# Optimization experiments

Hardware: AMD Instinct MI355X
Metric: run time of the kernel (lower is better)

Reference implementation:

```python
import jax, jax.numpy as jnp
import numpy as np

N_PEP, N_MHC, N_TCR = 20000, 5000, 100000
EMB, HID = 128, 256
E_PM, E_MT = 200000, 400000
B = 50000


def setup_inputs() -> dict:
    key = jax.random.key(0)
    ks = jax.random.split(key, 30)
    f32 = jnp.float32

    def w(k, shape, fan_in):
        # torch Linear default: U(-1/sqrt(fan_in), 1/sqrt(fan_in))
        lim = 1.0 / np.sqrt(fan_in)
        return jax.random.uniform(k, shape, dtype=f32, minval=-lim, maxval=lim)

    inp = {
        # embedding tables (learned params)
        "emb_pep": jax.random.normal(ks[0], (N_PEP, EMB), dtype=f32),
        "emb_mhc": jax.random.normal(ks[1], (N_MHC, EMB), dtype=f32),
        "emb_tcr": jax.random.normal(ks[2], (N_TCR, EMB), dtype=f32),
        # edge lists (src=edge_index[0], dst=edge_index[1])
        "src_pm": jax.random.randint(ks[3], (E_PM,), 0, N_PEP, dtype=jnp.int32),
        "dst_pm": jax.random.randint(ks[4], (E_PM,), 0, N_MHC, dtype=jnp.int32),
        "src_mt": jax.random.randint(ks[5], (E_MT,), 0, N_MHC, dtype=jnp.int32),
        "dst_mt": jax.random.randint(ks[6], (E_MT,), 0, N_TCR, dtype=jnp.int32),
        # triplet pack indices
        "pack_pep": jax.random.randint(ks[7], (B,), 0, N_PEP, dtype=jnp.int32),
        "pack_mhc": jax.random.randint(ks[8], (B,), 0, N_MHC, dtype=jnp.int32),
        "pack_tcr": jax.random.randint(ks[9], (B,), 0, N_TCR, dtype=jnp.int32),
        # SAGEConv params: Wl (aggregated neighbors, with bias), Wr (root, no bias)
        # layer 1: pep->mhc (src 128, dst 128); mhc->tcr (src 128, dst 128)
        "l1_pm_Wl": w(ks[10], (HID, EMB), EMB), "l1_pm_bl": w(ks[11], (HID,), EMB),
        "l1_pm_Wr": w(ks[12], (HID, EMB), EMB),
        "l1_mt_Wl": w(ks[13], (HID, EMB), EMB), "l1_mt_bl": w(ks[14], (HID,), EMB),
        "l1_mt_Wr": w(ks[15], (HID, EMB), EMB),
        # layer 2: pep->mhc (src 128, dst 256); mhc->tcr (src 256, dst 256)
        "l2_pm_Wl": w(ks[16], (HID, EMB), EMB), "l2_pm_bl": w(ks[17], (HID,), EMB),
        "l2_pm_Wr": w(ks[18], (HID, HID), HID),
        "l2_mt_Wl": w(ks[19], (HID, HID), HID), "l2_mt_bl": w(ks[20], (HID,), HID),
        "l2_mt_Wr": w(ks[21], (HID, HID), HID),
        # proj_pep and head MLP
        "proj_W": w(ks[22], (HID, EMB), EMB), "proj_b": w(ks[23], (HID,), EMB),
        "head_W1": w(ks[24], (HID, 3 * HID), 3 * HID), "head_b1": w(ks[25], (HID,), 3 * HID),
        "head_W2": w(ks[26], (1, HID), HID), "head_b2": w(ks[27], (1,), HID),
    }
    return inp


def _sage(x_src, x_dst, src, dst, Wl, bl, Wr, n_dst):
    # SAGEConv(mean): lin_l(mean_{j in N(i)} x_src[j]) + lin_r(x_dst[i])
    msg = jax.ops.segment_sum(x_src[src], dst, num_segments=n_dst)  # [n_dst, d_src]
    cnt = jax.ops.segment_sum(jnp.ones((src.shape[0],), x_src.dtype), dst, num_segments=n_dst)
    mean = msg / jnp.maximum(cnt, 1.0)[:, None]
    return mean @ Wl.T + bl + x_dst @ Wr.T


def reference(emb_pep, emb_mhc, emb_tcr,
              src_pm, dst_pm, src_mt, dst_mt,
              pack_pep, pack_mhc, pack_tcr,
              l1_pm_Wl, l1_pm_bl, l1_pm_Wr, l1_mt_Wl, l1_mt_bl, l1_mt_Wr,
              l2_pm_Wl, l2_pm_bl, l2_pm_Wr, l2_mt_Wl, l2_mt_bl, l2_mt_Wr,
              proj_W, proj_b, head_W1, head_b1, head_W2, head_b2):
    relu = jax.nn.relu
    # layer 1 (HeteroConv reads all relations from the same input dict)
    mhc1 = relu(_sage(emb_pep, emb_mhc, src_pm, dst_pm, l1_pm_Wl, l1_pm_bl, l1_pm_Wr, N_MHC))
    tcr1 = relu(_sage(emb_mhc, emb_tcr, src_mt, dst_mt, l1_mt_Wl, l1_mt_bl, l1_mt_Wr, N_TCR))
    # layer 2 ('pep' is never a destination, so it keeps its embedding)
    mhc2 = relu(_sage(emb_pep, mhc1, src_pm, dst_pm, l2_pm_Wl, l2_pm_bl, l2_pm_Wr, N_MHC))
    tcr2 = relu(_sage(mhc1, tcr1, src_mt, dst_mt, l2_mt_Wl, l2_mt_bl, l2_mt_Wr, N_TCR))
    # projections + triplet gather (dropout disabled: inference)
    hp = (emb_pep @ proj_W.T + proj_b)[pack_pep]  # [B, HID]
    hm = mhc2[pack_mhc]
    ht = tcr2[pack_tcr]
    z = jnp.concatenate([hp, hm, ht], axis=-1)  # [B, 3*HID]
    hidden = relu(z @ head_W1.T + head_b1)
    logits = hidden @ head_W2.T + head_b2
    return logits.squeeze(-1)
```

## Files before the change

### kernel.cpp

```cpp
#include <hip/hip_runtime.h>

constexpr int NPEP = 20000, NMHC = 5000, NTCR = 100000;
constexpr int EPM = 200000, EMT = 400000, BB = 50000;
constexpr int MAXU = 50000;

typedef __attribute__((ext_vector_type(8))) short bf16x8;
typedef __attribute__((ext_vector_type(4))) float f32x4;

__device__ inline ushort f2bf(float x) {
    union { float f; unsigned u; } v; v.f = x;
    unsigned r = (v.u + 0x7FFF + ((v.u >> 16) & 1)) >> 16;
    return (ushort)r;
}
__device__ inline float bf2f(ushort b) {
    union { unsigned u; float f; } t; t.u = ((unsigned)b) << 16; return t.f;
}
__device__ inline void bf2x2(unsigned u, float& a, float& b) {
    union { unsigned x; float f; } t1, t2;
    t1.x = u << 16; t2.x = u & 0xffff0000u;
    a = t1.f; b = t2.f;
}
__device__ inline ushort4 f4bf(float4 v) {
    return make_ushort4(f2bf(v.x), f2bf(v.y), f2bf(v.z), f2bf(v.w));
}

__global__ __launch_bounds__(256) void prep_kernel(
    int* __restrict__ ibz,
    const float4* __restrict__ Wr1f, ushort4* __restrict__ Wr1_b,
    const float4* __restrict__ Wr2f, ushort4* __restrict__ Wr2_b,
    const float* __restrict__ head_W1, ushort4* __restrict__ W1b_b, ushort4* __restrict__ W1c_b,
    const float* __restrict__ l1_pm_Wl, const float* __restrict__ l1_pm_Wr,
    const float* __restrict__ l1_mt_Wl, ushort* __restrict__ Wcat1_b,
    const float* __restrict__ l2_pm_Wl, const float* __restrict__ l2_pm_Wr,
    const float* __restrict__ l2_mt_Wl, ushort* __restrict__ Wcat2_b,
    const float4* __restrict__ emb_mhc, ushort* __restrict__ Acat1,
    const float* __restrict__ proj_W, const float* __restrict__ proj_b,
    ushort* __restrict__ Wcomp_b, float* __restrict__ bp) {
    __shared__ float red[128];
    const int b = blockIdx.x, tid = threadIdx.x;
    if (b < 303) {
        int i = b * 256 + tid;
        if (i < 77500) ((int4*)ibz)[i] = make_int4(0, 0, 0, 0);
    } else if (b < 335) {
        int i = (b - 303) * 256 + tid;
        if (i < 8192) Wr1_b[i] = f4bf(Wr1f[i]);
    } else if (b < 399) {
        int i = (b - 335) * 256 + tid;
        if (i < 16384) Wr2_b[i] = f4bf(Wr2f[i]);
    } else if (b < 463) {
        int i = (b - 399) * 256 + tid;
        if (i < 16384) {
            int n = i >> 6, k4 = (i & 63) * 4;
            float4 v = *(const float4*)(head_W1 + (size_t)n * 768 + 256 + k4);
            W1b_b[i] = f4bf(v);
        }
    } else if (b < 527) {
        int i = (b - 463) * 256 + tid;
        if (i < 16384) {
            int n = i >> 6, k4 = (i & 63) * 4;
            float4 v = *(const float4*)(head_W1 + (size_t)n * 768 + 512 + k4);
            W1c_b[i] = f4bf(v);
        }
    } else if (b < 1039) {
        int idx = (b - 527) * 256 + tid;
        if (idx < 131072) {
            int r = idx >> 8, k = idx & 255;
            float v;
            if (r < 256) v = (k < 128) ? l1_pm_Wl[r * 128 + k] : l1_pm_Wr[r * 128 + (k - 128)];
            else         v = (k < 128) ? 0.f : l1_mt_Wl[(r - 256) * 128 + (k - 128)];
            Wcat1_b[idx] = f2bf(v);
        }
    } else if (b < 1807) {
        int idx = (b - 1039) * 256 + tid;
        if (idx < 196608) {
            int r = idx / 384, k = idx - r * 384;
            float v;
            if (r < 256) v = (k < 128) ? l2_pm_Wl[r * 128 + k] : l2_pm_Wr[r * 256 + (k - 128)];
            else         v = (k < 128) ? 0.f : l2_mt_Wl[(r - 256) * 256 + (k - 128)];
            Wcat2_b[idx] = f2bf(v);
        }
    } else if (b < 2432) {
        int i4 = (b - 1807) * 256 + tid;
        if (i4 < 160000) {
            int r = i4 >> 5, c4 = (i4 & 31) * 4;
            *(ushort4*)(Acat1 + (size_t)r * 256 + 128 + c4) = f4bf(emb_mhc[i4]);
        }
    } else {
        int i = b - 2432;
        const float* w1row = head_W1 + (size_t)i * 768;
        if (tid < 128) {
            float acc = 0.f;
            for (int k = 0; k < 256; k++) acc += w1row[k] * proj_W[k * 128 + tid];
            Wcomp_b[i * 128 + tid] = f2bf(acc);
            float pb = w1row[2 * tid] * proj_b[2 * tid] + w1row[2 * tid + 1] * proj_b[2 * tid + 1];
            red[tid] = pb;
        }
        __syncthreads();
        if (tid < 64) { red[tid] += red[tid + 64]; }
        __syncthreads();
        if (tid < 32) { red[tid] += red[tid + 32]; }
        __syncthreads();
        if (tid == 0) {
            float s = 0.f;
            for (int j = 0; j < 32; j++) s += red[j];
            bp[i] = s;
        }
    }
}

__global__ void hist2_kernel(const int* __restrict__ dst_pm, const int* __restrict__ dst_mt,
                             const int* __restrict__ pack_tcr,
                             int* __restrict__ deg_pm, int* __restrict__ deg_mt,
                             int* __restrict__ mark) {
    int t = blockIdx.x * blockDim.x + threadIdx.x;
    if (t < EPM) atomicAdd(&deg_pm[dst_pm[t]], 1);
    else if (t < EPM + EMT) atomicAdd(&deg_mt[dst_mt[t - EPM]], 1);
    else if (t < EPM + EMT + BB) mark[pack_tcr[t - EPM - EMT]] = 1;
}

__global__ __launch_bounds__(256) void blocksum2_kernel(const int* __restrict__ deg_pm,
                                                        const int* __restrict__ deg_mt,
                                                        const int* __restrict__ mark,
                                                        int* __restrict__ bsum_pm,
                                                        int* __restrict__ bsum_mt,
                                                        int* __restrict__ bsum_mk) {
    __shared__ int red[256];
    const int tid = threadIdx.x;
    const int* deg; int n, bi; int* bsum;
    if (blockIdx.x < 5) { deg = deg_pm; n = NMHC; bi = blockIdx.x; bsum = bsum_pm; }
    else if (blockIdx.x < 103) { deg = deg_mt; n = NTCR; bi = blockIdx.x - 5; bsum = bsum_mt; }
    else { deg = mark; n = NTCR; bi = blockIdx.x - 103; bsum = bsum_mk; }
    const int base = bi * 1024;
    int s = 0;
#pragma unroll
    for (int j = 0; j < 4; j++) {
        int i = base + tid + j * 256;
        if (i < n) s += deg[i];
    }
    red[tid] = s;
    __syncthreads();
    for (int off = 128; off > 0; off >>= 1) {
        if (tid < off) red[tid] += red[tid + off];
        __syncthreads();
    }
    if (tid == 0) bsum[bi] = red[0];
}

__global__ __launch_bounds__(128) void scanb2_kernel(int* __restrict__ bsum_pm,
                                                     int* __restrict__ bsum_mt,
                                                     int* __restrict__ bsum_mk) {
    __shared__ int s[128];
    const int tid = threadIdx.x;
    int* bsum = (blockIdx.x == 0) ? bsum_pm : ((blockIdx.x == 1) ? bsum_mt : bsum_mk);
    const int nb = (blockIdx.x == 0) ? 5 : 98;
    int v = (tid < nb) ? bsum[tid] : 0;
    s[tid] = v;
    __syncthreads();
    for (int off = 1; off < 128; off <<= 1) {
        int t = (tid >= off) ? s[tid - off] : 0;
        __syncthreads();
        s[tid] += t;
        __syncthreads();
    }
    if (tid < nb) bsum[tid] = (tid > 0) ? s[tid - 1] : 0;
    if (tid == 0) bsum[nb] = s[nb - 1];
}

__global__ __launch_bounds__(256) void emit2_kernel(const int* __restrict__ deg_pm,
                                                    const int* __restrict__ deg_mt,
                                                    const int* __restrict__ mark,
                                                    const int* __restrict__ bsum_pm,
                                                    const int* __restrict__ bsum_mt,
                                                    const int* __restrict__ bsum_mk,
                                                    int* __restrict__ rp_pm, float* __restrict__ cnt_pm,
                                                    int* __restrict__ rp_mt, float* __restrict__ cnt_mt,
                                                    int* __restrict__ list) {
    __shared__ int tsum[256];
    const int tid = threadIdx.x;
    const int* deg; const int* bsum; int* rp; float* cnt; int n, nb, bi, mode;
    if (blockIdx.x < 5) { deg = deg_pm; bsum = bsum_pm; rp = rp_pm; cnt = cnt_pm; n = NMHC; nb = 5; bi = blockIdx.x; mode = 0; }
    else if (blockIdx.x < 103) { deg = deg_mt; bsum = bsum_mt; rp = rp_mt; cnt = cnt_mt; n = NTCR; nb = 98; bi = blockIdx.x - 5; mode = 0; }
    else { deg = mark; bsum = bsum_mk; rp = nullptr; cnt = nullptr; n = NTCR; nb = 98; bi = blockIdx.x - 103; mode = 1; }
    const int i0 = bi * 1024 + tid * 4;
    int4 v = make_int4(0, 0, 0, 0);
    if (i0 + 3 < n) v = *(const int4*)(deg + i0);
    else if (i0 < n) {
        int t[4] = {0, 0, 0, 0};
        for (int j = 0; j < 4 && i0 + j < n; j++) t[j] = deg[i0 + j];
        v = make_int4(t[0], t[1], t[2], t[3]);
    }
    int s = v.x + v.y + v.z + v.w;
    tsum[tid] = s;
    __syncthreads();
    for (int off = 1; off < 256; off <<= 1) {
        int t = (tid >= off) ? tsum[tid - off] : 0;
        __syncthreads();
        tsum[tid] += t;
        __syncthreads();
    }
    int ex = ((tid > 0) ? tsum[tid - 1] : 0) + bsum[bi];
    if (mode == 0) {
        if (i0 + 3 < n) {
            int r1 = ex + v.x, r2 = r1 + v.y, r3 = r2 + v.z;
            *(int4*)(rp + i0) = make_int4(ex, r1, r2, r3);
            *(float4*)(cnt + i0) = make_float4((float)v.x, (float)v.y, (float)v.z, (float)v.w);
        } else if (i0 < n) {
            int r = ex;
            int vv[4] = {v.x, v.y, v.z, v.w};
            for (int j = 0; j < 4 && i0 + j < n; j++) {
                rp[i0 + j] = r;
                cnt[i0 + j] = (float)vv[j];
                r += vv[j];
            }
        }
        if (bi == 0 && tid == 0) rp[n] = bsum[nb];
    } else {
        int p = ex;
        int vv[4] = {v.x, v.y, v.z, v.w};
#pragma unroll
        for (int j = 0; j < 4; j++) {
            if (i0 + j < n && vv[j]) list[p++] = i0 + j;
        }
    }
}

__global__ void fill2_kernel(const int* __restrict__ src_pm, const int* __restrict__ dst_pm,
                             const int* __restrict__ src_mt, const int* __restrict__ dst_mt,
                             const int* __restrict__ rp_pm, int* __restrict__ cur_pm, int* __restrict__ csr_pm,
                             const int* __restrict__ rp_mt, int* __restrict__ cur_mt, int* __restrict__ csr_mt) {
    int t = blockIdx.x * blockDim.x + threadIdx.x;
    if (t < EPM) {
        int d = dst_pm[t];
        int pos = atomicAdd(&cur_pm[d], 1);
        csr_pm[rp_pm[d] + pos] = src_pm[t];
    } else if (t < EPM + EMT) {
        int t2 = t - EPM;
        int d = dst_mt[t2];
        int pos = atomicAdd(&cur_mt[d], 1);
        csr_mt[rp_mt[d] + pos] = src_mt[t2];
    }
}

__global__ __launch_bounds__(256) void gatherpm_kernel(const int* __restrict__ rp,
                                                       const int* __restrict__ csr_src,
                                                       const float* __restrict__ X,
                                                       ushort* __restrict__ A1, ushort* __restrict__ A2,
                                                       int n) {
    const int tid = threadIdx.x;
    const int r = blockIdx.x * 8 + (tid >> 5);
    const int lane = tid & 31;
    if (r >= n) return;
    const int e0 = rp[r], e1 = rp[r + 1];
    float4 s = make_float4(0.f, 0.f, 0.f, 0.f);
    for (int e = e0; e < e1; e++) {
        const int sidx = csr_src[e];
        float4 v = ((const float4*)(X + (long)sidx * 128))[lane];
        s.x += v.x; s.y += v.y; s.z += v.z; s.w += v.w;
    }
    float sc = 1.f / fmaxf((float)(e1 - e0), 1.f);
    ushort4 o = make_ushort4(f2bf(s.x * sc), f2bf(s.y * sc), f2bf(s.z * sc), f2bf(s.w * sc));
    *(ushort4*)(A1 + (size_t)r * 256 + lane * 4) = o;
    *(ushort4*)(A2 + (size_t)r * 384 + lane * 4) = o;
}

template <int K, int NB0, bool RELU0, bool G2>
__global__ __launch_bounds__(256, 2) void mfma_fused_kernel(
    int M, const ushort* __restrict__ A, const ushort* __restrict__ W,
    const float* __restrict__ bias,
    ushort* __restrict__ out0, int s0, ushort* __restrict__ out1) {
    constexpr int RS = 40;
    __shared__ ushort Als[128 * RS];
    __shared__ ushort Wls[128 * RS];
    const int tid = threadIdx.x;
    const int m0 = blockIdx.x * 128, n0 = blockIdx.y * 128;
    const int lane = tid & 63, w = tid >> 6;
    const int wm = w >> 1, wn = w & 1;
    const int m16 = lane & 15, q = lane >> 4;

    f32x4 acc[4][4] = {};

    for (int k0 = 0; k0 < K; k0 += 32) {
        bf16x8 a_st[2], w_st[2];
#pragma unroll
        for (int r = 0; r < 2; r++) {
            int chunk = tid + r * 256;
            int row = chunk >> 2, off = (chunk & 3) * 8;
            int ga = min(m0 + row, M - 1);
            a_st[r] = *(const bf16x8*)(A + (size_t)ga * K + k0 + off);
            w_st[r] = *(const bf16x8*)(W + (size_t)(n0 + row) * K + k0 + off);
        }
        __syncthreads();
#pragma unroll
        for (int r = 0; r < 2; r++) {
            int chunk = tid + r * 256;
            int row = chunk >> 2, off = (chunk & 3) * 8;
            *(bf16x8*)(&Als[row * RS + off]) = a_st[r];
            *(bf16x8*)(&Wls[row * RS + off]) = w_st[r];
        }
        __syncthreads();
        bf16x8 af[4], bf[4];
#pragma unroll
        for (int t = 0; t < 4; t++) {
            af[t] = *(const bf16x8*)(&Als[(wm * 64 + t * 16 + m16) * RS + q * 8]);
            bf[t] = *(const bf16x8*)(&Wls[(wn * 64 + t * 16 + m16) * RS + q * 8]);
        }
#pragma unroll
        for (int mt = 0; mt < 4; mt++)
#pragma unroll
            for (int nt = 0; nt < 4; nt++)
                acc[mt][nt] = __builtin_amdgcn_mfma_f32_16x16x32_bf16(af[mt], bf[nt], acc[mt][nt], 0, 0, 0);
    }

    const bool g1 = G2 && ((int)blockIdx.y >= NB0);
#pragma unroll
    for (int mt = 0; mt < 4; mt++) {
#pragma unroll
        for (int i = 0; i < 4; i++) {
            int row = m0 + wm * 64 + mt * 16 + q * 4 + i;
            if (row >= M) continue;
#pragma unroll
            for (int nt = 0; nt < 4; nt++) {
                int col = n0 + wn * 64 + nt * 16 + m16;
                float v = acc[mt][nt][i];
                if (!g1) {
                    v += bias[col];
                    if (RELU0) v = fmaxf(v, 0.f);
                    out0[(size_t)row * s0 + col] = f2bf(v);
                } else {
                    out1[(size_t)row * 256 + (col - NB0 * 128)] = f2bf(v);
                }
            }
        }
    }
}

__global__ __launch_bounds__(256, 3) void tcrall_kernel(
    const int* __restrict__ nrowsp, const int* __restrict__ list,
    const int* __restrict__ rp, const int* __restrict__ csr_src,
    const ushort* __restrict__ Z1, const ushort* __restrict__ Z2,
    const float* __restrict__ emb_tcr,
    const ushort* __restrict__ Wr1, const ushort* __restrict__ Wr2,
    const ushort* __restrict__ W1c,
    const float* __restrict__ bl1, const float* __restrict__ bl2,
    ushort* __restrict__ Ht) {
    constexpr int RS1 = 136;
    constexpr int RS2 = 264;
    __shared__ ushort B[32 * RS2];
    __shared__ ushort A1[32 * RS2];
    __shared__ ushort A2[32 * RS2];
    __shared__ int origs[32];
    const int tid = threadIdx.x;
    const int M = nrowsp[0];
    const int m0 = blockIdx.x * 32;
    if (m0 >= M) return;
    const int lane = tid & 63, w = tid >> 6;
    const int m16 = lane & 15, q = lane >> 4;

    if (tid < 32) origs[tid] = list[min(m0 + tid, M - 1)];

#pragma unroll
    for (int r = 0; r < 4; r++) {
        int chunk = tid + r * 256;
        int row = chunk >> 5, c4 = (chunk & 31) * 4;
        int grow = list[min(m0 + row, M - 1)];
        float4 v = *(const float4*)(emb_tcr + (size_t)grow * 128 + c4);
        *(ushort4*)(&B[row * RS1 + c4]) = f4bf(v);
    }

    {
        const int g = tid >> 5, gl = tid & 31;
        for (int rr = g; rr < 32; rr += 8) {
            int cr = min(m0 + rr, M - 1);
            int orig = list[cr];
            int e0 = rp[orig], e1 = rp[orig + 1];
            float s1[8] = {}, s2[8] = {};
            for (int e = e0; e < e1; e++) {
                int sidx = csr_src[e];
                uint4 u1 = *(const uint4*)(Z1 + (size_t)sidx * 256 + gl * 8);
                uint4 u2 = *(const uint4*)(Z2 + (size_t)sidx * 256 + gl * 8);
                float a, b;
                bf2x2(u1.x, a, b); s1[0] += a; s1[1] += b;
                bf2x2(u1.y, a, b); s1[2] += a; s1[3] += b;
                bf2x2(u1.z, a, b); s1[4] += a; s1[5] += b;
                bf2x2(u1.w, a, b); s1[6] += a; s1[7] += b;
                bf2x2(u2.x, a, b); s2[0] += a; s2[1] += b;
                bf2x2(u2.y, a, b); s2[2] += a; s2[3] += b;
                bf2x2(u2.z, a, b); s2[4] += a; s2[5] += b;
                bf2x2(u2.w, a, b); s2[6] += a; s2[7] += b;
            }
            float es = 1.f / fmaxf((float)(e1 - e0), 1.f);
            uint4 w1, w2;
            w1.x = (unsigned)f2bf(s1[0] * es) | ((unsigned)f2bf(s1[1] * es) << 16);
            w1.y = (unsigned)f2bf(s1[2] * es) | ((unsigned)f2bf(s1[3] * es) << 16);
            w1.z = (unsigned)f2bf(s1[4] * es) | ((unsigned)f2bf(s1[5] * es) << 16);
            w1.w = (unsigned)f2bf(s1[6] * es) | ((unsigned)f2bf(s1[7] * es) << 16);
            w2.x = (unsigned)f2bf(s2[0] * es) | ((unsigned)f2bf(s2[1] * es) << 16);
            w2.y = (unsigned)f2bf(s2[2] * es) | ((unsigned)f2bf(s2[3] * es) << 16);
            w2.z = (unsigned)f2bf(s2[4] * es) | ((unsigned)f2bf(s2[5] * es) << 16);
            w2.w = (unsigned)f2bf(s2[6] * es) | ((unsigned)f2bf(s2[7] * es) << 16);
            *(uint4*)(&A1[rr * RS2 + gl * 8]) = w1;
            *(uint4*)(&A2[rr * RS2 + gl * 8]) = w2;
        }
    }
    __syncthreads();

    {
        f32x4 acc[2][4] = {};
        for (int k0 = 0; k0 < 128; k0 += 32) {
            bf16x8 af[2], bf[4];
#pragma unroll
            for (int t = 0; t < 2; t++)
                af[t] = *(const bf16x8*)(&B[(t * 16 + m16) * RS1 + k0 + q * 8]);
#pragma unroll
            for (int t = 0; t < 4; t++)
                bf[t] = *(const bf16x8*)(Wr1 + (size_t)(w * 64 + t * 16 + m16) * 128 + k0 + q * 8);
#pragma unroll
            for (int mt = 0; mt < 2; mt++)
#pragma unroll
                for (int nt = 0; nt < 4; nt++)
                    acc[mt][nt] = __builtin_amdgcn_mfma_f32_16x16x32_bf16(af[mt], bf[nt], acc[mt][nt], 0, 0, 0);
        }
        __syncthreads();
#pragma unroll
        for (int mt = 0; mt < 2; mt++)
#pragma unroll
            for (int i = 0; i < 4; i++) {
                int lr = mt * 16 + q * 4 + i;
#pragma unroll
                for (int nt = 0; nt < 4; nt++) {
                    int col = w * 64 + nt * 16 + m16;
                    float v = acc[mt][nt][i] + bl1[col] + bf2f(A1[lr * RS2 + col]);
                    B[lr * RS2 + col] = f2bf(fmaxf(v, 0.f));
                }
            }
    }
    __syncthreads();

    {
        f32x4 acc[2][4] = {};
        for (int k0 = 0; k0 < 256; k0 += 32) {
            bf16x8 af[2], bf[4];
#pragma unroll
            for (int t = 0; t < 2; t++)
                af[t] = *(const bf16x8*)(&B[(t * 16 + m16) * RS2 + k0 + q * 8]);
#pragma unroll
            for (int t = 0; t < 4; t++)
                bf[t] = *(const bf16x8*)(Wr2 + (size_t)(w * 64 + t * 16 + m16) * 256 + k0 + q * 8);
#pragma unroll
            for (int mt = 0; mt < 2; mt++)
#pragma unroll
                for (int nt = 0; nt < 4; nt++)
                    acc[mt][nt] = __builtin_amdgcn_mfma_f32_16x16x32_bf16(af[mt], bf[nt], acc[mt][nt], 0, 0, 0);
        }
        __syncthreads();
#pragma unroll
        for (int mt = 0; mt < 2; mt++)
#pragma unroll
            for (int i = 0; i < 4; i++) {
                int lr = mt * 16 + q * 4 + i;
#pragma unroll
                for (int nt = 0; nt < 4; nt++) {
                    int col = w * 64 + nt * 16 + m16;
                    float v = acc[mt][nt][i] + bl2[col] + bf2f(A2[lr * RS2 + col]);
                    B[lr * RS2 + col] = f2bf(fmaxf(v, 0.f));
                }
            }
    }
    __syncthreads();

    {
        f32x4 acc[2][4] = {};
        for (int k0 = 0; k0 < 256; k0 += 32) {
            bf16x8 af[2], bf[4];
#pragma unroll
            for (int t = 0; t < 2; t++)
                af[t] = *(const bf16x8*)(&B[(t * 16 + m16) * RS2 + k0 + q * 8]);
#pragma unroll
            for (int t = 0; t < 4; t++)
                bf[t] = *(const bf16x8*)(W1c + (size_t)(w * 64 + t * 16 + m16) * 256 + k0 + q * 8);
#pragma unroll
            for (int mt = 0; mt < 2; mt++)
#pragma unroll
                for (int nt = 0; nt < 4; nt++)
                    acc[mt][nt] = __builtin_amdgcn_mfma_f32_16x16x32_bf16(af[mt], bf[nt], acc[mt][nt], 0, 0, 0);
        }
        __syncthreads();
#pragma unroll
        for (int mt = 0; mt < 2; mt++)
#pragma unroll
            for (int i = 0; i < 4; i++) {
                int lr = mt * 16 + q * 4 + i;
#pragma unroll
                for (int nt = 0; nt < 4; nt++) {
                    int col = w * 64 + nt * 16 + m16;
                    B[lr * RS2 + col] = f2bf(acc[mt][nt][i]);
                }
            }
    }
    __syncthreads();

#pragma unroll
    for (int r = 0; r < 4; r++) {
        int chunk = tid + r * 256;
        int row = chunk >> 5, c8 = (chunk & 31) * 8;
        if (m0 + row < M)
            *(uint4*)(Ht + (size_t)origs[row] * 256 + c8) = *(const uint4*)(&B[row * RS2 + c8]);
    }
}

template <int K, bool HASB, bool AF32>
__global__ __launch_bounds__(256, 2) void mfma_out_kernel(
    int M, const void* __restrict__ Av, const ushort* __restrict__ W,
    const float* __restrict__ bias, ushort* __restrict__ out) {
    constexpr int RS = 40;
    __shared__ ushort Als[128 * RS];
    __shared__ ushort Wls[128 * RS];
    const int tid = threadIdx.x;
    const int m0 = blockIdx.x * 128, n0 = blockIdx.y * 128;
    const int lane = tid & 63, w = tid >> 6;
    const int wm = w >> 1, wn = w & 1;
    const int m16 = lane & 15, q = lane >> 4;

    f32x4 acc[4][4] = {};

    for (int k0 = 0; k0 < K; k0 += 32) {
        bf16x8 a_st[2], w_st[2];
#pragma unroll
        for (int r = 0; r < 2; r++) {
            int chunk = tid + r * 256;
            int row = chunk >> 2, off = (chunk & 3) * 8;
            int ga = min(m0 + row, M - 1);
            if constexpr (AF32) {
                const float* Af = (const float*)Av;
                float4 f0 = *(const float4*)(Af + (size_t)ga * K + k0 + off);
                float4 f1 = *(const float4*)(Af + (size_t)ga * K + k0 + off + 4);
                ushort4 u0 = f4bf(f0), u1 = f4bf(f1);
                bf16x8 av;
                av[0] = (short)u0.x; av[1] = (short)u0.y; av[2] = (short)u0.z; av[3] = (short)u0.w;
                av[4] = (short)u1.x; av[5] = (short)u1.y; av[6] = (short)u1.z; av[7] = (short)u1.w;
                a_st[r] = av;
            } else {
                a_st[r] = *(const bf16x8*)((const ushort*)Av + (size_t)ga * K + k0 + off);
            }
            w_st[r] = *(const bf16x8*)(W + (size_t)(n0 + row) * K + k0 + off);
        }
        __syncthreads();
#pragma unroll
        for (int r = 0; r < 2; r++) {
            int chunk = tid + r * 256;
            int row = chunk >> 2, off = (chunk & 3) * 8;
            *(bf16x8*)(&Als[row * RS + off]) = a_st[r];
            *(bf16x8*)(&Wls[row * RS + off]) = w_st[r];
        }
        __syncthreads();
        bf16x8 af[4], bf[4];
#pragma unroll
        for (int t = 0; t < 4; t++) {
            af[t] = *(const bf16x8*)(&Als[(wm * 64 + t * 16 + m16) * RS + q * 8]);
            bf[t] = *(const bf16x8*)(&Wls[(wn * 64 + t * 16 + m16) * RS + q * 8]);
        }
#pragma unroll
        for (int mt = 0; mt < 4; mt++)
#pragma unroll
            for (int nt = 0; nt < 4; nt++)
                acc[mt][nt] = __builtin_amdgcn_mfma_f32_16x16x32_bf16(af[mt], bf[nt], acc[mt][nt], 0, 0, 0);
    }

#pragma unroll
    for (int mt = 0; mt < 4; mt++) {
#pragma unroll
        for (int i = 0; i < 4; i++) {
            int row = m0 + wm * 64 + mt * 16 + q * 4 + i;
            if (row >= M) continue;
#pragma unroll
            for (int nt = 0; nt < 4; nt++) {
                int col = n0 + wn * 64 + nt * 16 + m16;
                float v = acc[mt][nt][i];
                if (HASB) v += bias[col];
                out[(size_t)row * 256 + col] = f2bf(v);
            }
        }
    }
}

__global__ __launch_bounds__(256) void combine_kernel(
    const ushort* __restrict__ Hp, const ushort* __restrict__ Hm, const ushort* __restrict__ Ht,
    const int* __restrict__ pp, const int* __restrict__ pm, const int* __restrict__ pt,
    const float* __restrict__ b1, const float* __restrict__ W2, const float* __restrict__ b2,
    float* __restrict__ out) {
    const int tid = threadIdx.x;
    const int lane = tid & 63, w = tid >> 6;
    const int c = lane * 4;
    const float4 b1v = *(const float4*)(b1 + c);
    const float4 w2v = *(const float4*)(W2 + c);
    const float b2v = b2[0];
    const int base = blockIdx.x * 32 + w * 8;
#pragma unroll
    for (int t = 0; t < 8; t++) {
        int i = base + t;
        if (i >= BB) return;
        int ra = pp[i], rb = pm[i], rc = pt[i];
        ushort4 ua = *(const ushort4*)(Hp + (size_t)ra * 256 + c);
        ushort4 ub = *(const ushort4*)(Hm + (size_t)rb * 256 + c);
        ushort4 uc = *(const ushort4*)(Ht + (size_t)rc * 256 + c);
        float h0 = fmaxf(bf2f(ua.x) + bf2f(ub.x) + bf2f(uc.x) + b1v.x, 0.f);
        float h1 = fmaxf(bf2f(ua.y) + bf2f(ub.y) + bf2f(uc.y) + b1v.y, 0.f);
        float h2 = fmaxf(bf2f(ua.z) + bf2f(ub.z) + bf2f(uc.z) + b1v.z, 0.f);
        float h3 = fmaxf(bf2f(ua.w) + bf2f(ub.w) + bf2f(uc.w) + b1v.w, 0.f);
        float p = h0 * w2v.x + h1 * w2v.y + h2 * w2v.z + h3 * w2v.w;
#pragma unroll
        for (int off = 32; off > 0; off >>= 1) p += __shfl_down(p, off);
        if (lane == 0) out[i] = p + b2v;
    }
}

extern "C" void kernel_launch(void* const* d_in, const int* in_sizes, int n_in,
                              void* d_out, int out_size, void* d_ws, size_t ws_size,
                              hipStream_t stream) {
    const float* emb_pep = (const float*)d_in[0];
    const float* emb_mhc = (const float*)d_in[1];
    const float* emb_tcr = (const float*)d_in[2];
    const int* src_pm = (const int*)d_in[3];
    const int* dst_pm = (const int*)d_in[4];
    const int* src_mt = (const int*)d_in[5];
    const int* dst_mt = (const int*)d_in[6];
    const int* pack_pep = (const int*)d_in[7];
    const int* pack_mhc = (const int*)d_in[8];
    const int* pack_tcr = (const int*)d_in[9];
    const float* l1_pm_Wl = (const float*)d_in[10];
    const float* l1_pm_bl = (const float*)d_in[11];
    const float* l1_pm_Wr = (const float*)d_in[12];
    const float* l1_mt_Wl = (const float*)d_in[13];
    const float* l1_mt_bl = (const float*)d_in[14];
    const float* l1_mt_Wr = (const float*)d_in[15];
    const float* l2_pm_Wl = (const float*)d_in[16];
    const float* l2_pm_bl = (const float*)d_in[17];
    const float* l2_pm_Wr = (const float*)d_in[18];
    const float* l2_mt_Wl = (const float*)d_in[19];
    const float* l2_mt_bl = (const float*)d_in[20];
    const float* l2_mt_Wr = (const float*)d_in[21];
    const float* proj_W = (const float*)d_in[22];
    const float* proj_b = (const float*)d_in[23];
    const float* head_W1 = (const float*)d_in[24];
    const float* head_b1 = (const float*)d_in[25];
    const float* head_W2 = (const float*)d_in[26];
    const float* head_b2 = (const float*)d_in[27];
    float* out = (float*)d_out;

    int* ib = (int*)d_ws;
    int* deg_pm = ib;
    int* cur_pm = ib + 5000;
    int* deg_mt = ib + 10000;
    int* cur_mt = ib + 110000;
    int* mark   = ib + 210000;
    int* rp_pm  = ib + 310000;
    int* rp_mt  = ib + 315008;
    int* csr_pm = ib + 415016;
    int* csr_mt = ib + 615016;
    int* bsum_pm = ib + 1015016;
    int* bsum_mt = ib + 1015176;
    int* bsum_mk = ib + 1015336;
    int* list    = ib + 1015496;

    float* f = (float*)(ib + 1065544);
    float* cnt_pm = f;
    float* cnt_mt = f + 5000;
    float* bp     = f + 105000;

    ushort* u = (ushort*)(f + 105344);
    ushort* Wcat1_b = u;
    ushort* Wcat2_b = u + 131072;
    ushort* W1b_b   = u + 327680;
    ushort* W1c_b   = u + 393216;
    ushort* Wcomp_b = u + 458752;
    ushort* Wr1_b   = u + 491520;
    ushort* Wr2_b   = u + 524288;
    ushort* Acat1   = u + 589824;
    ushort* Acat2   = u + 1869824;
    ushort* Zb1     = u + 3789824;
    ushort* Zb2     = u + 5069824;
    ushort* mhc2_b  = u + 6349824;
    ushort* Hp_b    = u + 7629824;
    ushort* Hm_b    = u + 12749824;
    ushort* Ht_b    = u + 14029824;

    prep_kernel<<<2688, 256, 0, stream>>>(
        ib,
        (const float4*)l1_mt_Wr, (ushort4*)Wr1_b,
        (const float4*)l2_mt_Wr, (ushort4*)Wr2_b,
        head_W1, (ushort4*)W1b_b, (ushort4*)W1c_b,
        l1_pm_Wl, l1_pm_Wr, l1_mt_Wl, Wcat1_b,
        l2_pm_Wl, l2_pm_Wr, l2_mt_Wl, Wcat2_b,
        (const float4*)emb_mhc, Acat1,
        proj_W, proj_b, Wcomp_b, bp);

    hist2_kernel<<<(EPM + EMT + BB + 255) / 256, 256, 0, stream>>>(
        dst_pm, dst_mt, pack_tcr, deg_pm, deg_mt, mark);
    blocksum2_kernel<<<201, 256, 0, stream>>>(deg_pm, deg_mt, mark, bsum_pm, bsum_mt, bsum_mk);
    scanb2_kernel<<<3, 128, 0, stream>>>(bsum_pm, bsum_mt, bsum_mk);
    emit2_kernel<<<201, 256, 0, stream>>>(deg_pm, deg_mt, mark, bsum_pm, bsum_mt, bsum_mk,
                                          rp_pm, cnt_pm, rp_mt, cnt_mt, list);
    fill2_kernel<<<(EPM + EMT + 255) / 256, 256, 0, stream>>>(
        src_pm, dst_pm, src_mt, dst_mt, rp_pm, cur_pm, csr_pm, rp_mt, cur_mt, csr_mt);

    gatherpm_kernel<<<(NMHC + 7) / 8, 256, 0, stream>>>(rp_pm, csr_pm, emb_pep, Acat1, Acat2, NMHC);

    mfma_fused_kernel<256, 2, true, true><<<dim3((NMHC + 127) / 128, 4), 256, 0, stream>>>(
        NMHC, Acat1, Wcat1_b, l1_pm_bl, Acat2 + 128, 384, Zb1);
    mfma_fused_kernel<384, 2, true, true><<<dim3((NMHC + 127) / 128, 4), 256, 0, stream>>>(
        NMHC, Acat2, Wcat2_b, l2_pm_bl, mhc2_b, 256, Zb2);

    tcrall_kernel<<<(MAXU + 31) / 32, 256, 0, stream>>>(
        bsum_mk + 98, list, rp_mt, csr_mt, Zb1, Zb2, emb_tcr,
        Wr1_b, Wr2_b, W1c_b, l1_mt_bl, l2_mt_bl, Ht_b);

    mfma_out_kernel<128, true, true><<<dim3((NPEP + 127) / 128, 2), 256, 0, stream>>>(
        NPEP, emb_pep, Wcomp_b, bp, Hp_b);
    mfma_out_kernel<256, false, false><<<dim3((NMHC + 127) / 128, 2), 256, 0, stream>>>(
        NMHC, mhc2_b, W1b_b, nullptr, Hm_b);

    combine_kernel<<<(BB + 31) / 32, 256, 0, stream>>>(
        Hp_b, Hm_b, Ht_b, pack_pep, pack_mhc, pack_tcr,
        head_b1, head_W2, head_b2, out);
}
```

Before: 416.3 us.

## Fuse triplet head combine into TCR kernel via per-TCR batch CSR

Builds a CSR that maps each unique packed TCR row to the batch entries referencing it, by counting pack_tcr multiplicities and adding inverse and row-pointer arrays to the scan. The TCR kernel then finishes the head MLP directly from its shared-memory TCR projection, gathering Hp and Hm per batch entry and writing logits. This removes the Ht intermediate round trip and the separate combine kernel launch. In exchange it adds atomics to the CSR build and makes the per-row loop length uneven across waves, which can cause imbalance.

```diff
diff --git a/kernel.cpp b/kernel.cpp
--- a/kernel.cpp
+++ b/kernel.cpp
@@ -38,31 +38,31 @@
     ushort* __restrict__ Wcomp_b, float* __restrict__ bp) {
     __shared__ float red[128];
     const int b = blockIdx.x, tid = threadIdx.x;
-    if (b < 303) {
+    if (b < 352) {
         int i = b * 256 + tid;
-        if (i < 77500) ((int4*)ibz)[i] = make_int4(0, 0, 0, 0);
-    } else if (b < 335) {
-        int i = (b - 303) * 256 + tid;
+        if (i < 90000) ((int4*)ibz)[i] = make_int4(0, 0, 0, 0);
+    } else if (b < 384) {
+        int i = (b - 352) * 256 + tid;
         if (i < 8192) Wr1_b[i] = f4bf(Wr1f[i]);
-    } else if (b < 399) {
-        int i = (b - 335) * 256 + tid;
+    } else if (b < 448) {
+        int i = (b - 384) * 256 + tid;
         if (i < 16384) Wr2_b[i] = f4bf(Wr2f[i]);
-    } else if (b < 463) {
-        int i = (b - 399) * 256 + tid;
+    } else if (b < 512) {
+        int i = (b - 448) * 256 + tid;
         if (i < 16384) {
             int n = i >> 6, k4 = (i & 63) * 4;
             float4 v = *(const float4*)(head_W1 + (size_t)n * 768 + 256 + k4);
             W1b_b[i] = f4bf(v);
         }
-    } else if (b < 527) {
-        int i = (b - 463) * 256 + tid;
+    } else if (b < 576) {
+        int i = (b - 512) * 256 + tid;
         if (i < 16384) {
             int n = i >> 6, k4 = (i & 63) * 4;
             float4 v = *(const float4*)(head_W1 + (size_t)n * 768 + 512 + k4);
             W1c_b[i] = f4bf(v);
         }
-    } else if (b < 1039) {
-        int idx = (b - 527) * 256 + tid;
+    } else if (b < 1088) {
+        int idx = (b - 576) * 256 + tid;
         if (idx < 131072) {
             int r = idx >> 8, k = idx & 255;
             float v;
@@ -70,8 +70,8 @@
             else         v = (k < 128) ? 0.f : l1_mt_Wl[(r - 256) * 128 + (k - 128)];
             Wcat1_b[idx] = f2bf(v);
         }
-    } else if (b < 1807) {
-        int idx = (b - 1039) * 256 + tid;
+    } else if (b < 1856) {
+        int idx = (b - 1088) * 256 + tid;
         if (idx < 196608) {
             int r = idx / 384, k = idx - r * 384;
             float v;
@@ -79,14 +79,14 @@
             else         v = (k < 128) ? 0.f : l2_mt_Wl[(r - 256) * 256 + (k - 128)];
             Wcat2_b[idx] = f2bf(v);
         }
-    } else if (b < 2432) {
-        int i4 = (b - 1807) * 256 + tid;
+    } else if (b < 2481) {
+        int i4 = (b - 1856) * 256 + tid;
         if (i4 < 160000) {
             int r = i4 >> 5, c4 = (i4 & 31) * 4;
             *(ushort4*)(Acat1 + (size_t)r * 256 + 128 + c4) = f4bf(emb_mhc[i4]);
         }
     } else {
-        int i = b - 2432;
+        int i = b - 2481;
         const float* w1row = head_W1 + (size_t)i * 768;
         if (tid < 128) {
             float acc = 0.f;
@@ -111,47 +111,56 @@
 __global__ void hist2_kernel(const int* __restrict__ dst_pm, const int* __restrict__ dst_mt,
                              const int* __restrict__ pack_tcr,
                              int* __restrict__ deg_pm, int* __restrict__ deg_mt,
-                             int* __restrict__ mark) {
+                             int* __restrict__ degT) {
     int t = blockIdx.x * blockDim.x + threadIdx.x;
     if (t < EPM) atomicAdd(&deg_pm[dst_pm[t]], 1);
     else if (t < EPM + EMT) atomicAdd(&deg_mt[dst_mt[t - EPM]], 1);
-    else if (t < EPM + EMT + BB) mark[pack_tcr[t - EPM - EMT]] = 1;
+    else if (t < EPM + EMT + BB) atomicAdd(&degT[pack_tcr[t - EPM - EMT]], 1);
 }
 
 __global__ __launch_bounds__(256) void blocksum2_kernel(const int* __restrict__ deg_pm,
                                                         const int* __restrict__ deg_mt,
-                                                        const int* __restrict__ mark,
+                                                        const int* __restrict__ degT,
                                                         int* __restrict__ bsum_pm,
                                                         int* __restrict__ bsum_mt,
-                                                        int* __restrict__ bsum_mk) {
+                                                        int* __restrict__ bsum_mk,
+                                                        int* __restrict__ bsum_mk2) {
     __shared__ int red[256];
+    __shared__ int redc[256];
     const int tid = threadIdx.x;
-    const int* deg; int n, bi; int* bsum;
-    if (blockIdx.x < 5) { deg = deg_pm; n = NMHC; bi = blockIdx.x; bsum = bsum_pm; }
-    else if (blockIdx.x < 103) { deg = deg_mt; n = NTCR; bi = blockIdx.x - 5; bsum = bsum_mt; }
-    else { deg = mark; n = NTCR; bi = blockIdx.x - 103; bsum = bsum_mk; }
+    const int* deg; int n, bi; int mk = 0;
+    if (blockIdx.x < 5) { deg = deg_pm; n = NMHC; bi = blockIdx.x; }
+    else if (blockIdx.x < 103) { deg = deg_mt; n = NTCR; bi = blockIdx.x - 5; }
+    else { deg = degT; n = NTCR; bi = blockIdx.x - 103; mk = 1; }
     const int base = bi * 1024;
-    int s = 0;
+    int s = 0, sc = 0;
 #pragma unroll
     for (int j = 0; j < 4; j++) {
         int i = base + tid + j * 256;
-        if (i < n) s += deg[i];
-    }
-    red[tid] = s;
+        if (i < n) { int d = deg[i]; s += d; sc += (d != 0); }
+    }
+    red[tid] = s; redc[tid] = sc;
     __syncthreads();
     for (int off = 128; off > 0; off >>= 1) {
-        if (tid < off) red[tid] += red[tid + off];
-        __syncthreads();
-    }
-    if (tid == 0) bsum[bi] = red[0];
+        if (tid < off) { red[tid] += red[tid + off]; redc[tid] += redc[tid + off]; }
+        __syncthreads();
+    }
+    if (tid == 0) {
+        if (mk) { bsum_mk[bi] = redc[0]; bsum_mk2[bi] = red[0]; }
+        else if (blockIdx.x < 5) bsum_pm[bi] = red[0];
+        else bsum_mt[bi] = red[0];
+    }
 }
 
 __global__ __launch_bounds__(128) void scanb2_kernel(int* __restrict__ bsum_pm,
                                                      int* __restrict__ bsum_mt,
-                                                     int* __restrict__ bsum_mk) {
+                                                     int* __restrict__ bsum_mk,
+                                                     int* __restrict__ bsum_mk2) {
     __shared__ int s[128];
     const int tid = threadIdx.x;
-    int* bsum = (blockIdx.x == 0) ? bsum_pm : ((blockIdx.x == 1) ? bsum_mt : bsum_mk);
+    int* bsum = (blockIdx.x == 0) ? bsum_pm
+              : (blockIdx.x == 1) ? bsum_mt
+              : (blockIdx.x == 2) ? bsum_mk : bsum_mk2;
     const int nb = (blockIdx.x == 0) ? 5 : 98;
     int v = (tid < nb) ? bsum[tid] : 0;
     s[tid] = v;
@@ -168,19 +177,22 @@
 
 __global__ __launch_bounds__(256) void emit2_kernel(const int* __restrict__ deg_pm,
                                                     const int* __restrict__ deg_mt,
-                                                    const int* __restrict__ mark,
+                                                    const int* __restrict__ degT,
                                                     const int* __restrict__ bsum_pm,
                                                     const int* __restrict__ bsum_mt,
                                                     const int* __restrict__ bsum_mk,
+                                                    const int* __restrict__ bsum_mk2,
                                                     int* __restrict__ rp_pm, float* __restrict__ cnt_pm,
                                                     int* __restrict__ rp_mt, float* __restrict__ cnt_mt,
-                                                    int* __restrict__ list) {
+                                                    int* __restrict__ list, int* __restrict__ inv,
+                                                    int* __restrict__ rpT) {
     __shared__ int tsum[256];
+    __shared__ int tcnt[256];
     const int tid = threadIdx.x;
     const int* deg; const int* bsum; int* rp; float* cnt; int n, nb, bi, mode;
     if (blockIdx.x < 5) { deg = deg_pm; bsum = bsum_pm; rp = rp_pm; cnt = cnt_pm; n = NMHC; nb = 5; bi = blockIdx.x; mode = 0; }
     else if (blockIdx.x < 103) { deg = deg_mt; bsum = bsum_mt; rp = rp_mt; cnt = cnt_mt; n = NTCR; nb = 98; bi = blockIdx.x - 5; mode = 0; }
-    else { deg = mark; bsum = bsum_mk; rp = nullptr; cnt = nullptr; n = NTCR; nb = 98; bi = blockIdx.x - 103; mode = 1; }
+    else { deg = degT; bsum = bsum_mk; rp = nullptr; cnt = nullptr; n = NTCR; nb = 98; bi = blockIdx.x - 103; mode = 1; }
     const int i0 = bi * 1024 + tid * 4;
     int4 v = make_int4(0, 0, 0, 0);
     if (i0 + 3 < n) v = *(const int4*)(deg + i0);
@@ -189,17 +201,18 @@
         for (int j = 0; j < 4 && i0 + j < n; j++) t[j] = deg[i0 + j];
         v = make_int4(t[0], t[1], t[2], t[3]);
     }
-    int s = v.x + v.y + v.z + v.w;
-    tsum[tid] = s;
+    tsum[tid] = v.x + v.y + v.z + v.w;
+    tcnt[tid] = (v.x != 0) + (v.y != 0) + (v.z != 0) + (v.w != 0);
     __syncthreads();
     for (int off = 1; off < 256; off <<= 1) {
-        int t = (tid >= off) ? tsum[tid - off] : 0;
-        __syncthreads();
-        tsum[tid] += t;
-        __syncthreads();
-    }
-    int ex = ((tid > 0) ? tsum[tid - 1] : 0) + bsum[bi];
+        int tB = (tid >= off) ? tsum[tid - off] : 0;
+        int tA = (tid >= off) ? tcnt[tid - off] : 0;
+        __syncthreads();
+        tsum[tid] += tB; tcnt[tid] += tA;
+        __syncthreads();
+    }
     if (mode == 0) {
+        int ex = ((tid > 0) ? tsum[tid - 1] : 0) + bsum[bi];
         if (i0 + 3 < n) {
             int r1 = ex + v.x, r2 = r1 + v.y, r3 = r2 + v.z;
             *(int4*)(rp + i0) = make_int4(ex, r1, r2, r3);
@@ -215,19 +228,29 @@
         }
         if (bi == 0 && tid == 0) rp[n] = bsum[nb];
     } else {
-        int p = ex;
+        int p  = ((tid > 0) ? tcnt[tid - 1] : 0) + bsum_mk[bi];
+        int e2 = ((tid > 0) ? tsum[tid - 1] : 0) + bsum_mk2[bi];
         int vv[4] = {v.x, v.y, v.z, v.w};
 #pragma unroll
         for (int j = 0; j < 4; j++) {
-            if (i0 + j < n && vv[j]) list[p++] = i0 + j;
-        }
+            if (i0 + j < n && vv[j]) {
+                list[p] = i0 + j;
+                inv[i0 + j] = p;
+                rpT[p] = e2;
+                p++; e2 += vv[j];
+            }
+        }
+        if (bi == 0 && tid == 0) rpT[bsum_mk[nb]] = BB;
     }
 }
 
 __global__ void fill2_kernel(const int* __restrict__ src_pm, const int* __restrict__ dst_pm,
                              const int* __restrict__ src_mt, const int* __restrict__ dst_mt,
+                             const int* __restrict__ pack_tcr,
                              const int* __restrict__ rp_pm, int* __restrict__ cur_pm, int* __restrict__ csr_pm,
-                             const int* __restrict__ rp_mt, int* __restrict__ cur_mt, int* __restrict__ csr_mt) {
+                             const int* __restrict__ rp_mt, int* __restrict__ cur_mt, int* __restrict__ csr_mt,
+                             const int* __restrict__ inv, const int* __restrict__ rpT,
+                             int* __restrict__ curT, int* __restrict__ csrT) {
     int t = blockIdx.x * blockDim.x + threadIdx.x;
     if (t < EPM) {
         int d = dst_pm[t];
@@ -238,6 +261,11 @@
         int d = dst_mt[t2];
         int pos = atomicAdd(&cur_mt[d], 1);
         csr_mt[rp_mt[d] + pos] = src_mt[t2];
+    } else if (t < EPM + EMT + BB) {
+        int t2 = t - EPM - EMT;
+        int crow = inv[pack_tcr[t2]];
+        int pos = atomicAdd(&curT[crow], 1);
+        csrT[rpT[crow] + pos] = t2;
     }
 }
 
@@ -342,21 +370,22 @@
     const ushort* __restrict__ Wr1, const ushort* __restrict__ Wr2,
     const ushort* __restrict__ W1c,
     const float* __restrict__ bl1, const float* __restrict__ bl2,
-    ushort* __restrict__ Ht) {
+    const int* __restrict__ rpT, const int* __restrict__ csrT,
+    const ushort* __restrict__ Hp, const ushort* __restrict__ Hm,
+    const int* __restrict__ pp, const int* __restrict__ pm,
+    const float* __restrict__ b1, const float* __restrict__ W2,
+    const float* __restrict__ b2, float* __restrict__ out) {
     constexpr int RS1 = 136;
     constexpr int RS2 = 264;
     __shared__ ushort B[32 * RS2];
     __shared__ ushort A1[32 * RS2];
     __shared__ ushort A2[32 * RS2];
-    __shared__ int origs[32];
     const int tid = threadIdx.x;
     const int M = nrowsp[0];
     const int m0 = blockIdx.x * 32;
     if (m0 >= M) return;
     const int lane = tid & 63, w = tid >> 6;
     const int m16 = lane & 15, q = lane >> 4;
-
-    if (tid < 32) origs[tid] = list[min(m0 + tid, M - 1)];
 
 #pragma unroll
     for (int r = 0; r < 4; r++) {
@@ -499,12 +528,33 @@
     }
     __syncthreads();
 
-#pragma unroll
-    for (int r = 0; r < 4; r++) {
-        int chunk = tid + r * 256;
-        int row = chunk >> 5, c8 = (chunk & 31) * 8;
-        if (m0 + row < M)
-            *(uint4*)(Ht + (size_t)origs[row] * 256 + c8) = *(const uint4*)(&B[row * RS2 + c8]);
+    {
+        const int c = lane * 4;
+        const float4 b1v = *(const float4*)(b1 + c);
+        const float4 w2v = *(const float4*)(W2 + c);
+        const float b2v = b2[0];
+        const int nrow = min(32, M - m0);
+        for (int lr = w; lr < nrow; lr += 4) {
+            const int crow = m0 + lr;
+            const int t0 = rpT[crow], t1 = rpT[crow + 1];
+            ushort4 uc = *(const ushort4*)(&B[lr * RS2 + c]);
+            const float c0 = bf2f(uc.x) + b1v.x, c1 = bf2f(uc.y) + b1v.y;
+            const float c2 = bf2f(uc.z) + b1v.z, c3 = bf2f(uc.w) + b1v.w;
+            for (int e = t0; e < t1; e++) {
+                const int i = csrT[e];
+                const int ra = pp[i], rb = pm[i];
+                ushort4 ua = *(const ushort4*)(Hp + (size_t)ra * 256 + c);
+                ushort4 ub = *(const ushort4*)(Hm + (size_t)rb * 256 + c);
+                float h0 = fmaxf(bf2f(ua.x) + bf2f(ub.x) + c0, 0.f);
+                float h1 = fmaxf(bf2f(ua.y) + bf2f(ub.y) + c1, 0.f);
+                float h2 = fmaxf(bf2f(ua.z) + bf2f(ub.z) + c2, 0.f);
+                float h3 = fmaxf(bf2f(ua.w) + bf2f(ub.w) + c3, 0.f);
+                float p = h0 * w2v.x + h1 * w2v.y + h2 * w2v.z + h3 * w2v.w;
+#pragma unroll
+                for (int off = 32; off > 0; off >>= 1) p += __shfl_down(p, off);
+                if (lane == 0) out[i] = p + b2v;
+            }
+        }
     }
 }
 
@@ -580,37 +630,6 @@
                 out[(size_t)row * 256 + col] = f2bf(v);
             }
         }
-    }
-}
-
-__global__ __launch_bounds__(256) void combine_kernel(
-    const ushort* __restrict__ Hp, const ushort* __restrict__ Hm, const ushort* __restrict__ Ht,
-    const int* __restrict__ pp, const int* __restrict__ pm, const int* __restrict__ pt,
-    const float* __restrict__ b1, const float* __restrict__ W2, const float* __restrict__ b2,
-    float* __restrict__ out) {
-    const int tid = threadIdx.x;
-    const int lane = tid & 63, w = tid >> 6;
-    const int c = lane * 4;
-    const float4 b1v = *(const float4*)(b1 + c);
-    const float4 w2v = *(const float4*)(W2 + c);
-    const float b2v = b2[0];
-    const int base = blockIdx.x * 32 + w * 8;
-#pragma unroll
-    for (int t = 0; t < 8; t++) {
-        int i = base + t;
-        if (i >= BB) return;
-        int ra = pp[i], rb = pm[i], rc = pt[i];
-        ushort4 ua = *(const ushort4*)(Hp + (size_t)ra * 256 + c);
-        ushort4 ub = *(const ushort4*)(Hm + (size_t)rb * 256 + c);
-        ushort4 uc = *(const ushort4*)(Ht + (size_t)rc * 256 + c);
-        float h0 = fmaxf(bf2f(ua.x) + bf2f(ub.x) + bf2f(uc.x) + b1v.x, 0.f);
-        float h1 = fmaxf(bf2f(ua.y) + bf2f(ub.y) + bf2f(uc.y) + b1v.y, 0.f);
-        float h2 = fmaxf(bf2f(ua.z) + bf2f(ub.z) + bf2f(uc.z) + b1v.z, 0.f);
-        float h3 = fmaxf(bf2f(ua.w) + bf2f(ub.w) + bf2f(uc.w) + b1v.w, 0.f);
-        float p = h0 * w2v.x + h1 * w2v.y + h2 * w2v.z + h3 * w2v.w;
-#pragma unroll
-        for (int off = 32; off > 0; off >>= 1) p += __shfl_down(p, off);
-        if (lane == 0) out[i] = p + b2v;
     }
 }
 
@@ -652,17 +671,22 @@
     int* cur_pm = ib + 5000;
     int* deg_mt = ib + 10000;
     int* cur_mt = ib + 110000;
-    int* mark   = ib + 210000;
-    int* rp_pm  = ib + 310000;
-    int* rp_mt  = ib + 315008;
-    int* csr_pm = ib + 415016;
-    int* csr_mt = ib + 615016;
-    int* bsum_pm = ib + 1015016;
-    int* bsum_mt = ib + 1015176;
-    int* bsum_mk = ib + 1015336;
-    int* list    = ib + 1015496;
-
-    float* f = (float*)(ib + 1065544);
+    int* degT   = ib + 210000;
+    int* curT   = ib + 310000;
+    int* rp_pm  = ib + 360000;
+    int* rp_mt  = ib + 365008;
+    int* csr_pm = ib + 465016;
+    int* csr_mt = ib + 665016;
+    int* bsum_pm = ib + 1065016;
+    int* bsum_mt = ib + 1065176;
+    int* bsum_mk = ib + 1065336;
+    int* bsum_mk2 = ib + 1065496;
+    int* list    = ib + 1065656;
+    int* inv     = ib + 1115704;
+    int* rpT     = ib + 1215704;
+    int* csrT    = ib + 1265760;
+
+    float* f = (float*)(ib + 1315760);
     float* cnt_pm = f;
     float* cnt_mt = f + 5000;
     float* bp     = f + 105000;
@@ -682,9 +706,8 @@
     ushort* mhc2_b  = u + 6349824;
     ushort* Hp_b    = u + 7629824;
     ushort* Hm_b    = u + 12749824;
-    ushort* Ht_b    = u + 14029824;
-
-    prep_kernel<<<2688, 256, 0, stream>>>(
+
+    prep_kernel<<<2737, 256, 0, stream>>>(
         ib,
         (const float4*)l1_mt_Wr, (ushort4*)Wr1_b,
         (const float4*)l2_mt_Wr, (ushort4*)Wr2_b,
@@ -695,13 +718,17 @@
         proj_W, proj_b, Wcomp_b, bp);
 
     hist2_kernel<<<(EPM + EMT + BB + 255) / 256, 256, 0, stream>>>(
-        dst_pm, dst_mt, pack_tcr, deg_pm, deg_mt, mark);
-    blocksum2_kernel<<<201, 256, 0, stream>>>(deg_pm, deg_mt, mark, bsum_pm, bsum_mt, bsum_mk);
-    scanb2_kernel<<<3, 128, 0, stream>>>(bsum_pm, bsum_mt, bsum_mk);
-    emit2_kernel<<<201, 256, 0, stream>>>(deg_pm, deg_mt, mark, bsum_pm, bsum_mt, bsum_mk,
-                                          rp_pm, cnt_pm, rp_mt, cnt_mt, list);
-    fill2_kernel<<<(EPM + EMT + 255) / 256, 256, 0, stream>>>(
-        src_pm, dst_pm, src_mt, dst_mt, rp_pm, cur_pm, csr_pm, rp_mt, cur_mt, csr_mt);
+        dst_pm, dst_mt, pack_tcr, deg_pm, deg_mt, degT);
+    blocksum2_kernel<<<201, 256, 0, stream>>>(deg_pm, deg_mt, degT,
+                                              bsum_pm, bsum_mt, bsum_mk, bsum_mk2);
+    scanb2_kernel<<<4, 128, 0, stream>>>(bsum_pm, bsum_mt, bsum_mk, bsum_mk2);
+    emit2_kernel<<<201, 256, 0, stream>>>(deg_pm, deg_mt, degT,
+                                          bsum_pm, bsum_mt, bsum_mk, bsum_mk2,
+                                          rp_pm, cnt_pm, rp_mt, cnt_mt, list, inv, rpT);
+    fill2_kernel<<<(EPM + EMT + BB + 255) / 256, 256, 0, stream>>>(
+        src_pm, dst_pm, src_mt, dst_mt, pack_tcr,
+        rp_pm, cur_pm, csr_pm, rp_mt, cur_mt, csr_mt,
+        inv, rpT, curT, csrT);
 
     gatherpm_kernel<<<(NMHC + 7) / 8, 256, 0, stream>>>(rp_pm, csr_pm, emb_pep, Acat1, Acat2, NMHC);
 
@@ -710,16 +737,14 @@
     mfma_fused_kernel<384, 2, true, true><<<dim3((NMHC + 127) / 128, 4), 256, 0, stream>>>(
         NMHC, Acat2, Wcat2_b, l2_pm_bl, mhc2_b, 256, Zb2);
 
-    tcrall_kernel<<<(MAXU + 31) / 32, 256, 0, stream>>>(
-        bsum_mk + 98, list, rp_mt, csr_mt, Zb1, Zb2, emb_tcr,
-        Wr1_b, Wr2_b, W1c_b, l1_mt_bl, l2_mt_bl, Ht_b);
-
     mfma_out_kernel<128, true, true><<<dim3((NPEP + 127) / 128, 2), 256, 0, stream>>>(
         NPEP, emb_pep, Wcomp_b, bp, Hp_b);
     mfma_out_kernel<256, false, false><<<dim3((NMHC + 127) / 128, 2), 256, 0, stream>>>(
         NMHC, mhc2_b, W1b_b, nullptr, Hm_b);
 
-    combine_kernel<<<(BB + 31) / 32, 256, 0, stream>>>(
-        Hp_b, Hm_b, Ht_b, pack_pep, pack_mhc, pack_tcr,
+    tcrall_kernel<<<(MAXU + 31) / 32, 256, 0, stream>>>(
+        bsum_mk + 98, list, rp_mt, csr_mt, Zb1, Zb2, emb_tcr,
+        Wr1_b, Wr2_b, W1c_b, l1_mt_bl, l2_mt_bl,
+        rpT, csrT, Hp_b, Hm_b, pack_pep, pack_mhc,
         head_b1, head_W2, head_b2, out);
 }
```

After: 434.2 us. 4.3% more time.
